# Optimization experiments

Hardware: AMD Instinct MI355X
Metric: run time of the kernel (lower is better)

## Reference

```python
import jax, jax.numpy as jnp
import numpy as np

D = 768; H = 12; T = 8; E = 4; L = 197; B = 4; BT = B * T


def _ln(x, g, b):
    m = x.mean(-1, keepdims=True)
    v = ((x - m) ** 2).mean(-1, keepdims=True)
    return (x - m) / jnp.sqrt(v + 1e-5) * g + b


def _qgelu(x):
    return x * jax.nn.sigmoid(1.702 * x)


def _mha(x, wqkv, bqkv, wo, bo):
    # x: (L, N, D), torch nn.MultiheadAttention semantics (seq-first)
    Lx, N, Dm = x.shape
    hd = Dm // H
    qkv = x @ wqkv.T + bqkv                      # (L, N, 3D)
    q, k, v = jnp.split(qkv, 3, axis=-1)
    sh = lambda t: t.reshape(Lx, N, H, hd).transpose(1, 2, 0, 3)  # (N,H,L,hd)
    q, k, v = sh(q), sh(k), sh(v)
    att = jax.nn.softmax(jnp.einsum('nhld,nhmd->nhlm', q, k) / np.sqrt(hd).astype(np.float32), -1)
    o = jnp.einsum('nhlm,nhmd->nhld', att, v).transpose(2, 0, 1, 3).reshape(Lx, N, Dm)
    return o @ wo.T + bo


def setup_inputs() -> dict:
    key = jax.random.key(0)
    ks = iter(jax.random.split(key, 40))
    s = 0.02
    p = {}
    p['x'] = jax.random.normal(next(ks), (L, BT, D), jnp.float32)
    p['msg_fc_w'] = s * jax.random.normal(next(ks), (D, D)); p['msg_fc_b'] = jnp.zeros((D,))
    p['msg_ln_g'] = jnp.ones((D,)); p['msg_ln_b'] = jnp.zeros((D,))
    p['msg_attn_wqkv'] = s * jax.random.normal(next(ks), (3 * D, D)); p['msg_attn_bqkv'] = jnp.zeros((3 * D,))
    p['msg_attn_wo'] = s * jax.random.normal(next(ks), (D, D)); p['msg_attn_bo'] = jnp.zeros((D,))
    p['attn_wqkv'] = s * jax.random.normal(next(ks), (3 * D, D)); p['attn_bqkv'] = jnp.zeros((3 * D,))
    p['attn_wo'] = s * jax.random.normal(next(ks), (D, D)); p['attn_bo'] = jnp.zeros((D,))
    p['ln1_g'] = jnp.ones((D,)); p['ln1_b'] = jnp.zeros((D,))
    p['ln2_g'] = jnp.ones((D,)); p['ln2_b'] = jnp.zeros((D,))
    p['cfc_w'] = s * jax.random.normal(next(ks), (4 * D, D)); p['cfc_b'] = jnp.zeros((4 * D,))
    p['cproj_w'] = s * jax.random.normal(next(ks), (D, 4 * D)); p['cproj_b'] = jnp.zeros((D,))
    p['eh_w'] = s * jax.random.normal(next(ks), (E, 4 * D, D)); p['eh_b'] = jnp.zeros((E, 4 * D))
    p['et_w'] = s * jax.random.normal(next(ks), (E, D, 4 * D)); p['et_b'] = jnp.zeros((E, D))
    p['r1_w'] = s * jax.random.normal(next(ks), (E + 1, D)); p['r1_b'] = jnp.zeros((E + 1,))
    p['r2_w'] = s * jax.random.normal(next(ks), (E + 1, 4 * D)); p['r2_b'] = jnp.zeros((E + 1,))
    return p


def reference(x, msg_fc_w, msg_fc_b, msg_ln_g, msg_ln_b, msg_attn_wqkv, msg_attn_bqkv,
              msg_attn_wo, msg_attn_bo, attn_wqkv, attn_bqkv, attn_wo, attn_bo,
              ln1_g, ln1_b, ln2_g, ln2_b, cfc_w, cfc_b, cproj_w, cproj_b,
              eh_w, eh_b, et_w, et_b, r1_w, r1_b, r2_w, r2_b):
    l, bt, d = x.shape
    b = bt // T
    x4 = x.reshape(l, b, T, d)
    # message token from CLS (position 0) of each frame
    msg = x4[0] @ msg_fc_w.T + msg_fc_b          # (b, T, d)
    msg = msg.transpose(1, 0, 2)                 # (T, b, d) - attend across frames
    mln = _ln(msg, msg_ln_g, msg_ln_b)
    msg = msg + _mha(mln, msg_attn_wqkv, msg_attn_bqkv, msg_attn_wo, msg_attn_bo)
    msg_r = msg.transpose(1, 0, 2)[None]         # (1, b, T, d)
    xc = jnp.concatenate([x4, msg_r], axis=0).reshape(l + 1, bt, d)
    xc = xc + _mha(_ln(xc, ln1_g, ln1_b), attn_wqkv, attn_bqkv, attn_wo, attn_bo)
    x = xc[:l]
    ln_x = _ln(x, ln2_g, ln2_b)
    # soft-MoE head: shared c_fc is expert 0, then E expert heads
    Wh = jnp.concatenate([cfc_w[None], eh_w], 0)     # (E+1, 4D, D)
    bh = jnp.concatenate([cfc_b[None], eh_b], 0)     # (E+1, 4D)
    heads = jnp.einsum('lbd,efd->lbef', ln_x, Wh) + bh  # (l, bt, E+1, 4D)
    r1 = jax.nn.softmax(ln_x @ r1_w.T + r1_b, -1)       # (l, bt, E+1)
    oh = jnp.einsum('lbe,lbef->lbf', r1, heads)
    oh = _qgelu(oh)
    # soft-MoE tail
    Wt = jnp.concatenate([cproj_w[None], et_w], 0)   # (E+1, D, 4D)
    btl = jnp.concatenate([cproj_b[None], et_b], 0)  # (E+1, D)
    tails = jnp.einsum('lbf,edf->lbed', oh, Wt) + btl  # (l, bt, E+1, D)
    r2 = jax.nn.softmax(oh @ r2_w.T + r2_b, -1)
    out = jnp.einsum('lbe,lbed->lbd', r2, tails)
    return x + out
```

## Files before the change

kernel.cpp:

```cpp
#include <hip/hip_runtime.h>
#include <hip/hip_bf16.h>

typedef __hip_bfloat16 bf16;
typedef __attribute__((ext_vector_type(8))) short short8;
typedef __attribute__((ext_vector_type(4))) float f32x4;

__device__ __forceinline__ float b2f(bf16 v){ return __bfloat162float(v); }
__device__ __forceinline__ unsigned short f2bits(float v){
  bf16 h = __float2bfloat16(v);
  return *reinterpret_cast<unsigned short*>(&h);
}

__device__ __forceinline__ void gload16(const bf16* g, bf16* l){
  __builtin_amdgcn_global_load_lds((const __attribute__((address_space(1))) void*)g,
                                   (__attribute__((address_space(3))) void*)l, 16, 0, 0);
}

__device__ __forceinline__ void ld4(const float* p, float& a,float& b,float& c,float& d){
  float4 v = *reinterpret_cast<const float4*>(p); a=v.x; b=v.y; c=v.z; d=v.w;
}
__device__ __forceinline__ float wave_sum(float v){
  #pragma unroll
  for (int off=32; off>0; off>>=1) v += __shfl_down(v, off);
  return v;
}

__global__ __launch_bounds__(256) void prep_weights(
    const float* __restrict__ s0, const float* __restrict__ s1,
    const float* __restrict__ s2, const float* __restrict__ s3,
    const float* __restrict__ s4, const float* __restrict__ s5,
    bf16* __restrict__ d0, bf16* __restrict__ d1, bf16* __restrict__ d2,
    bf16* __restrict__ d3, bf16* __restrict__ d4, bf16* __restrict__ d5){
  long i4 = (long)blockIdx.x*256 + threadIdx.x;
  const float* s; bf16* d; long base;
  if      (i4 <  442368){ s=s0; d=d0; base=0; }
  else if (i4 <  589824){ s=s1; d=d1; base=442368; }
  else if (i4 < 1179648){ s=s2; d=d2; base=589824; }
  else if (i4 < 3538944){ s=s3; d=d3; base=1179648; }
  else if (i4 < 4128768){ s=s4; d=d4; base=3538944; }
  else                  { s=s5; d=d5; base=4128768; }
  long j = (i4 - base)*4;
  float4 v = *reinterpret_cast<const float4*>(s + j);
  d[j]   = __float2bfloat16(v.x);
  d[j+1] = __float2bfloat16(v.y);
  d[j+2] = __float2bfloat16(v.z);
  d[j+3] = __float2bfloat16(v.w);
}

__global__ __launch_bounds__(256) void prep_bias(
    const float* __restrict__ cfc_b, const float* __restrict__ eh_b,
    const float* __restrict__ cproj_b, const float* __restrict__ et_b,
    float* __restrict__ bias_h, float* __restrict__ bias_t){
  int i = blockIdx.x*256 + threadIdx.x;
  if (i < 3072)       bias_h[i] = cfc_b[i];
  else if (i < 15360) bias_h[i] = eh_b[i-3072];
  else if (i < 16128) bias_t[i-15360] = cproj_b[i-15360];
  else if (i < 19200) bias_t[i-15360] = et_b[i-16128];
}

__global__ __launch_bounds__(256) void ln_rows(const float* __restrict__ in,
    const float* __restrict__ g, const float* __restrict__ b,
    float* __restrict__ out){
  int row = blockIdx.x;
  const float* x = in + (size_t)row*768;
  float* o = out + (size_t)row*768;
  float s=0.f, s2=0.f;
  for (int d=threadIdx.x; d<768; d+=256){ float v=x[d]; s+=v; s2+=v*v; }
  s = wave_sum(s); s2 = wave_sum(s2);
  __shared__ float red[8];
  __shared__ float stat[2];
  int lane = threadIdx.x & 63, wid = threadIdx.x >> 6;
  if (lane==0){ red[wid]=s; red[4+wid]=s2; }
  __syncthreads();
  if (threadIdx.x==0){
    float S=red[0]+red[1]+red[2]+red[3];
    float S2=red[4]+red[5]+red[6]+red[7];
    float m = S*(1.f/768.f);
    float var = S2*(1.f/768.f) - m*m;
    stat[0]=m; stat[1]=rsqrtf(var + 1e-5f);
  }
  __syncthreads();
  float m=stat[0], inv=stat[1];
  for (int d=threadIdx.x; d<768; d+=256)
    o[d] = (x[d]-m)*inv*g[d] + b[d];
}

__global__ __launch_bounds__(256) void ln_rows_b(const float* __restrict__ in,
    const float* __restrict__ g, const float* __restrict__ b,
    bf16* __restrict__ out){
  int row = blockIdx.x;
  const float* x = in + (size_t)row*768;
  bf16* o = out + (size_t)row*768;
  float s=0.f, s2=0.f;
  for (int d=threadIdx.x; d<768; d+=256){ float v=x[d]; s+=v; s2+=v*v; }
  s = wave_sum(s); s2 = wave_sum(s2);
  __shared__ float red[8];
  __shared__ float stat[2];
  int lane = threadIdx.x & 63, wid = threadIdx.x >> 6;
  if (lane==0){ red[wid]=s; red[4+wid]=s2; }
  __syncthreads();
  if (threadIdx.x==0){
    float S=red[0]+red[1]+red[2]+red[3];
    float S2=red[4]+red[5]+red[6]+red[7];
    float m = S*(1.f/768.f);
    float var = S2*(1.f/768.f) - m*m;
    stat[0]=m; stat[1]=rsqrtf(var + 1e-5f);
  }
  __syncthreads();
  float m=stat[0], inv=stat[1];
  for (int d=threadIdx.x; d<768; d+=256)
    o[d] = __float2bfloat16((x[d]-m)*inv*g[d] + b[d]);
}

template<int K>
__global__ __launch_bounds__(256) void router2(const bf16* __restrict__ X,
    const float* __restrict__ W, const float* __restrict__ bias,
    float* __restrict__ out, int rows){
  int row = blockIdx.x*4 + (threadIdx.x>>6);
  int lane = threadIdx.x & 63;
  if (row >= rows) return;
  const bf16* x = X + (size_t)row*K;
  constexpr int NC = K/64;
  float xa[NC];
  #pragma unroll
  for (int c=0;c<NC;++c) xa[c] = b2f(x[c*64 + lane]);
  float lg[5];
  #pragma unroll
  for (int e=0;e<5;++e){
    const float* w = W + (size_t)e*K;
    float p=0.f;
    #pragma unroll
    for (int c=0;c<NC;++c) p += xa[c]*w[c*64 + lane];
    lg[e] = wave_sum(p);
  }
  if (lane==0){
    float mx=-1e30f;
    #pragma unroll
    for (int e=0;e<5;++e){ lg[e] += bias[e]; mx = fmaxf(mx, lg[e]); }
    float s=0.f;
    #pragma unroll
    for (int e=0;e<5;++e){ lg[e]=expf(lg[e]-mx); s+=lg[e]; }
    float inv=1.f/s;
    #pragma unroll
    for (int e=0;e<5;++e) out[(size_t)row*5+e] = lg[e]*inv;
  }
}

__global__ __launch_bounds__(64) void msg_attn(const float* __restrict__ mqkv,
    float* __restrict__ mattno){
  int bh = blockIdx.x; int b = bh/12, h = bh%12;
  __shared__ float qs[8][64], ks[8][64], vs[8][64], sc[8][8];
  int lane = threadIdx.x;
  for (int i=lane; i<512; i+=64){
    int t=i>>6, d=i&63;
    size_t base = ((size_t)(b*8+t))*2304 + h*64 + d;
    qs[t][d]=mqkv[base]; ks[t][d]=mqkv[base+768]; vs[t][d]=mqkv[base+1536];
  }
  __syncthreads();
  { int t=lane>>3, m=lane&7; float a=0.f;
    #pragma unroll
    for (int d=0;d<64;++d) a += qs[t][d]*ks[m][d];
    sc[t][m] = a*0.125f; }
  __syncthreads();
  if (lane<8){
    int t=lane; float mx=-1e30f;
    #pragma unroll
    for (int m=0;m<8;++m) mx=fmaxf(mx, sc[t][m]);
    float s=0.f;
    #pragma unroll
    for (int m=0;m<8;++m){ float e=expf(sc[t][m]-mx); sc[t][m]=e; s+=e; }
    float inv=1.f/s;
    #pragma unroll
    for (int m=0;m<8;++m) sc[t][m]*=inv;
  }
  __syncthreads();
  { int t=lane>>3, d0=(lane&7)*8;
    for (int dd=0; dd<8; ++dd){
      int d=d0+dd; float a=0.f;
      #pragma unroll
      for (int m=0;m<8;++m) a += sc[t][m]*vs[m][d];
      mattno[((size_t)(b*8+t))*768 + h*64 + d] = a;
    } }
}

__global__ __launch_bounds__(256) void attn_mfma(const bf16* __restrict__ qkv,
    bf16* __restrict__ attno){
  constexpr int KP = 232;
  __shared__ __align__(16) unsigned short Ks[208*72];
  __shared__ __align__(16) unsigned short Vt[64*KP];
  __shared__ __align__(16) unsigned short Ps[4*16*KP];

  int tid = threadIdx.x;
  int bh = blockIdx.x; int bb = bh/12, h = bh%12;
  int l0 = blockIdx.y*64;
  int wv = tid>>6, ln = tid&63, quad = ln>>4, mrow = ln&15;

  for (int i=tid; i<1584; i+=256){
    int m=i>>3, dc=(i&7)<<3;
    const uint4 kv = *reinterpret_cast<const uint4*>(qkv + ((size_t)(m*32+bb))*2304 + 768 + h*64 + dc);
    *reinterpret_cast<uint4*>(Ks + m*72 + dc) = kv;
    const uint4 vv = *reinterpret_cast<const uint4*>(qkv + ((size_t)(m*32+bb))*2304 + 1536 + h*64 + dc);
    unsigned int w[4] = {vv.x, vv.y, vv.z, vv.w};
    #pragma unroll
    for (int j=0;j<4;++j){
      Vt[(dc+2*j  )*KP + m] = (unsigned short)(w[j] & 0xffff);
      Vt[(dc+2*j+1)*KP + m] = (unsigned short)(w[j] >> 16);
    }
  }
  for (int i=tid; i<10*72; i+=256) Ks[198*72 + i] = 0;
  for (int i=tid; i<64*34; i+=256){ int d=i/34, c=198+(i%34); Vt[d*KP+c] = 0; }
  { unsigned int* pz = reinterpret_cast<unsigned int*>(Ps);
    for (int i=tid; i<4*16*KP/2; i+=256) pz[i] = 0; }

  int ql = l0 + wv*16 + mrow;
  short8 aq[2] = { {0,0,0,0,0,0,0,0}, {0,0,0,0,0,0,0,0} };
  if (ql < 198){
    aq[0] = *reinterpret_cast<const short8*>(qkv + ((size_t)(ql*32+bb))*2304 + h*64 + quad*8);
    aq[1] = *reinterpret_cast<const short8*>(qkv + ((size_t)(ql*32+bb))*2304 + h*64 + 32 + quad*8);
  }
  __syncthreads();

  f32x4 sc[13];
  const f32x4 zero = {0.f,0.f,0.f,0.f};
  #pragma unroll
  for (int t=0;t<13;++t){
    const short8 bk0 = *reinterpret_cast<const short8*>(Ks + (t*16+mrow)*72 + quad*8);
    const short8 bk1 = *reinterpret_cast<const short8*>(Ks + (t*16+mrow)*72 + 32 + quad*8);
    f32x4 a = zero;
    a = __builtin_amdgcn_mfma_f32_16x16x32_bf16(aq[0], bk0, a, 0,0,0);
    a = __builtin_amdgcn_mfma_f32_16x16x32_bf16(aq[1], bk1, a, 0,0,0);
    sc[t] = a * 0.125f;
  }
  if (192 + mrow >= 198) sc[12] = (f32x4){-1e30f,-1e30f,-1e30f,-1e30f};

  float inv[4];
  #pragma unroll
  for (int r=0;r<4;++r){
    float m = -1e30f;
    #pragma unroll
    for (int t=0;t<13;++t) m = fmaxf(m, sc[t][r]);
    #pragma unroll
    for (int msk=1; msk<16; msk<<=1) m = fmaxf(m, __shfl_xor(m, msk));
    float s = 0.f;
    #pragma unroll
    for (int t=0;t<13;++t){ float e = __expf(sc[t][r]-m); sc[t][r]=e; s+=e; }
    #pragma unroll
    for (int msk=1; msk<16; msk<<=1) s += __shfl_xor(s, msk);
    inv[r] = 1.f/s;
  }

  #pragma unroll
  for (int t=0;t<13;++t)
    #pragma unroll
    for (int r=0;r<4;++r)
      Ps[(wv*16 + quad*4+r)*KP + t*16+mrow] = f2bits(sc[t][r]);
  __syncthreads();

  f32x4 o[4] = {zero,zero,zero,zero};
  #pragma unroll
  for (int kc=0;kc<7;++kc){
    const short8 ap = *reinterpret_cast<const short8*>(Ps + (wv*16+mrow)*KP + kc*32 + quad*8);
    #pragma unroll
    for (int nt=0;nt<4;++nt){
      const short8 bv = *reinterpret_cast<const short8*>(Vt + (nt*16+mrow)*KP + kc*32 + quad*8);
      o[nt] = __builtin_amdgcn_mfma_f32_16x16x32_bf16(ap, bv, o[nt], 0,0,0);
    }
  }
  #pragma unroll
  for (int r=0;r<4;++r){
    int l = l0 + wv*16 + quad*4 + r;
    if (l >= 198) continue;
    #pragma unroll
    for (int nt=0;nt<4;++nt){
      int d = nt*16 + mrow;
      attno[((size_t)(l*32+bb))*768 + h*64 + d] = __float2bfloat16(o[nt][r]*inv[r]);
    }
  }
}

__global__ __launch_bounds__(256) void gemm_nt(const float* __restrict__ A,
    const float* __restrict__ B, const float* __restrict__ bias,
    const float* res, float* C,
    int M, int N, int K){
  __shared__ __align__(16) float As[16][68];
  __shared__ __align__(16) float Bs[16][68];
  int tid=threadIdx.x, tx=tid&15, ty=tid>>4;
  int row0=blockIdx.y*64, col0=blockIdx.x*64;
  int lrow=tid>>2, lk4=(tid&3)*4;
  float acc[4][4]={};
  for (int kb=0; kb<K; kb+=16){
    int gr = row0 + lrow;
    if (gr < M){
      float a0,a1,a2,a3; ld4(A + (size_t)gr*K + kb + lk4, a0,a1,a2,a3);
      As[lk4][lrow]=a0; As[lk4+1][lrow]=a1; As[lk4+2][lrow]=a2; As[lk4+3][lrow]=a3;
    } else {
      As[lk4][lrow]=0.f; As[lk4+1][lrow]=0.f; As[lk4+2][lrow]=0.f; As[lk4+3][lrow]=0.f;
    }
    { float c0,c1,c2,c3; ld4(B + (size_t)(col0+lrow)*K + kb + lk4, c0,c1,c2,c3);
      Bs[lk4][lrow]=c0; Bs[lk4+1][lrow]=c1; Bs[lk4+2][lrow]=c2; Bs[lk4+3][lrow]=c3; }
    __syncthreads();
    #pragma unroll
    for (int kk=0;kk<16;++kk){
      float4 a4 = *reinterpret_cast<const float4*>(&As[kk][ty*4]);
      float4 b4 = *reinterpret_cast<const float4*>(&Bs[kk][tx*4]);
      float av[4]={a4.x,a4.y,a4.z,a4.w};
      float bw[4]={b4.x,b4.y,b4.z,b4.w};
      #pragma unroll
      for (int u=0;u<4;++u)
        #pragma unroll
        for (int v=0;v<4;++v) acc[u][v] += av[u]*bw[v];
    }
    __syncthreads();
  }
  #pragma unroll
  for (int u=0;u<4;++u){
    int gi = row0 + ty*4 + u;
    if (gi >= M) continue;
    #pragma unroll
    for (int v=0;v<4;++v){
      int gj = col0 + tx*4 + v;
      float r = res ? res[(size_t)gi*N+gj] : 0.f;
      float bb = bias ? bias[gj] : 0.f;
      C[(size_t)gi*N+gj] = r + acc[u][v] + bb;
    }
  }
}

template<int MODE>
__global__ __launch_bounds__(256,3) void gemm_mfma(
    const bf16* __restrict__ A, const bf16* __restrict__ B,
    const float* __restrict__ bias,
    const float* res, float* __restrict__ outf,
    bf16* __restrict__ outb, int M, int N, int K)
{
  __shared__ __align__(16) bf16 As0[4096];
  __shared__ __align__(16) bf16 As1[4096];
  __shared__ __align__(16) bf16 Bs0[4096];
  __shared__ __align__(16) bf16 Bs1[4096];

  int tid=threadIdx.x, wv=tid>>6, ln=tid&63;
  int quad=ln>>4, mrow=ln&15;
  int row0=blockIdx.y*128, col0=blockIdx.x*128;
  int wr=wv>>1, wc=wv&1;

  int c0 = wv*64 + ln;
  int r0 = c0>>2, cc=(c0&3)*8;

  int aoff[4], boff[4];
  #pragma unroll
  for (int i=0;i<4;++i){
    aoff[i] = (wr*64 + i*16 + mrow)*32 + quad*8;
    boff[i] = (wc*64 + i*16 + mrow)*32 + quad*8;
  }

  f32x4 acc[4][4];
  const f32x4 zero = {0.f,0.f,0.f,0.f};
  #pragma unroll
  for (int i=0;i<4;++i)
    #pragma unroll
    for (int j=0;j<4;++j) acc[i][j]=zero;

  const bf16* Ab = A + (size_t)(row0+r0)*K + cc;
  const bf16* Bb = B + (size_t)(col0+r0)*K + cc;
  for (int kb=0; kb<K; kb+=64){
    gload16(Ab + kb,                As0 + wv*512);
    gload16(Ab + (size_t)64*K + kb, As0 + 2048 + wv*512);
    gload16(Bb + kb,                Bs0 + wv*512);
    gload16(Bb + (size_t)64*K + kb, Bs0 + 2048 + wv*512);
    gload16(Ab + kb + 32,                As1 + wv*512);
    gload16(Ab + (size_t)64*K + kb + 32, As1 + 2048 + wv*512);
    gload16(Bb + kb + 32,                Bs1 + wv*512);
    gload16(Bb + (size_t)64*K + kb + 32, Bs1 + 2048 + wv*512);
    __syncthreads();
    short8 af[4], bfr[4];
    #pragma unroll
    for (int i=0;i<4;++i) af[i]  = *reinterpret_cast<const short8*>(As0 + aoff[i]);
    #pragma unroll
    for (int j=0;j<4;++j) bfr[j] = *reinterpret_cast<const short8*>(Bs0 + boff[j]);
    #pragma unroll
    for (int i=0;i<4;++i)
      #pragma unroll
      for (int j=0;j<4;++j)
        acc[i][j] = __builtin_amdgcn_mfma_f32_16x16x32_bf16(af[i], bfr[j], acc[i][j], 0, 0, 0);
    #pragma unroll
    for (int i=0;i<4;++i) af[i]  = *reinterpret_cast<const short8*>(As1 + aoff[i]);
    #pragma unroll
    for (int j=0;j<4;++j) bfr[j] = *reinterpret_cast<const short8*>(Bs1 + boff[j]);
    #pragma unroll
    for (int i=0;i<4;++i)
      #pragma unroll
      for (int j=0;j<4;++j)
        acc[i][j] = __builtin_amdgcn_mfma_f32_16x16x32_bf16(af[i], bfr[j], acc[i][j], 0, 0, 0);
    __syncthreads();
  }

  #pragma unroll
  for (int i=0;i<4;++i){
    #pragma unroll
    for (int r=0;r<4;++r){
      int gi = row0 + wr*64 + i*16 + quad*4 + r;
      if (gi >= M) continue;
      #pragma unroll
      for (int j=0;j<4;++j){
        int gj = col0 + wc*64 + j*16 + mrow;
        if (MODE==0) outb[(size_t)gi*N+gj] = __float2bfloat16(acc[i][j][r] + bias[gj]);
        else         outf[(size_t)gi*N+gj] = acc[i][j][r] + bias[gj] + res[(size_t)gi*N+gj];
      }
    }
  }
}

template<int MODE>
__global__ __launch_bounds__(256,2) void gemm_moe(
    const bf16* __restrict__ A, const bf16* __restrict__ B,
    const float* __restrict__ bias, const float* __restrict__ rmat,
    const float* __restrict__ res, float* __restrict__ outf,
    bf16* __restrict__ outb, int M, int N, int K)
{
  __shared__ __align__(16) bf16 As0[4096];
  __shared__ __align__(16) bf16 As1[4096];
  __shared__ __align__(16) bf16 Bs0[4096];
  __shared__ __align__(16) bf16 Bs1[4096];

  int tid=threadIdx.x, wv=tid>>6, ln=tid&63;
  int quad=ln>>4, mrow=ln&15;
  int row0=blockIdx.y*128, col0=blockIdx.x*128;
  int wr=wv>>1, wc=wv&1;

  int c0 = wv*64 + ln;
  int r0 = c0>>2, cc=(c0&3)*8;

  int aoff[4], boff[4];
  #pragma unroll
  for (int i=0;i<4;++i){
    aoff[i] = (wr*64 + i*16 + mrow)*32 + quad*8;
    boff[i] = (wc*64 + i*16 + mrow)*32 + quad*8;
  }

  const f32x4 zero = {0.f,0.f,0.f,0.f};
  f32x4 fin[4][4];
  #pragma unroll
  for (int i=0;i<4;++i)
    #pragma unroll
    for (int j=0;j<4;++j) fin[i][j]=zero;

  const bf16* Ab = A + (size_t)(row0+r0)*K + cc;

  for (int e=0; e<5; ++e){
    f32x4 acc[4][4];
    #pragma unroll
    for (int i=0;i<4;++i)
      #pragma unroll
      for (int j=0;j<4;++j) acc[i][j]=zero;

    const bf16* Bb = B + (size_t)e*N*K + (size_t)(col0+r0)*K + cc;
    for (int kb=0; kb<K; kb+=64){
      gload16(Ab + kb,                As0 + wv*512);
      gload16(Ab + (size_t)64*K + kb, As0 + 2048 + wv*512);
      gload16(Bb + kb,                Bs0 + wv*512);
      gload16(Bb + (size_t)64*K + kb, Bs0 + 2048 + wv*512);
      gload16(Ab + kb + 32,                As1 + wv*512);
      gload16(Ab + (size_t)64*K + kb + 32, As1 + 2048 + wv*512);
      gload16(Bb + kb + 32,                Bs1 + wv*512);
      gload16(Bb + (size_t)64*K + kb + 32, Bs1 + 2048 + wv*512);
      __syncthreads();
      short8 af[4], bfr[4];
      #pragma unroll
      for (int i=0;i<4;++i) af[i]  = *reinterpret_cast<const short8*>(As0 + aoff[i]);
      #pragma unroll
      for (int j=0;j<4;++j) bfr[j] = *reinterpret_cast<const short8*>(Bs0 + boff[j]);
      #pragma unroll
      for (int i=0;i<4;++i)
        #pragma unroll
        for (int j=0;j<4;++j)
          acc[i][j] = __builtin_amdgcn_mfma_f32_16x16x32_bf16(af[i], bfr[j], acc[i][j], 0, 0, 0);
      #pragma unroll
      for (int i=0;i<4;++i) af[i]  = *reinterpret_cast<const short8*>(As1 + aoff[i]);
      #pragma unroll
      for (int j=0;j<4;++j) bfr[j] = *reinterpret_cast<const short8*>(Bs1 + boff[j]);
      #pragma unroll
      for (int i=0;i<4;++i)
        #pragma unroll
        for (int j=0;j<4;++j)
          acc[i][j] = __builtin_amdgcn_mfma_f32_16x16x32_bf16(af[i], bfr[j], acc[i][j], 0, 0, 0);
      __syncthreads();
    }

    float bv[4];
    #pragma unroll
    for (int j=0;j<4;++j) bv[j] = bias[e*N + col0 + wc*64 + j*16 + mrow];
    #pragma unroll
    for (int i=0;i<4;++i){
      #pragma unroll
      for (int r=0;r<4;++r){
        int gi = row0 + wr*64 + i*16 + quad*4 + r;
        float w = (gi < M) ? rmat[(size_t)gi*5 + e] : 0.f;
        #pragma unroll
        for (int j=0;j<4;++j)
          fin[i][j][r] += w * (acc[i][j][r] + bv[j]);
      }
    }
  }

  #pragma unroll
  for (int i=0;i<4;++i){
    #pragma unroll
    for (int r=0;r<4;++r){
      int gi = row0 + wr*64 + i*16 + quad*4 + r;
      if (gi >= M) continue;
      #pragma unroll
      for (int j=0;j<4;++j){
        int gj = col0 + wc*64 + j*16 + mrow;
        float v = fin[i][j][r];
        if (MODE==0){
          float q = v / (1.f + __expf(-1.702f*v));
          outb[(size_t)gi*N+gj] = __float2bfloat16(q);
        } else {
          outf[(size_t)gi*N+gj] = v + res[(size_t)gi*N+gj];
        }
      }
    }
  }
}

extern "C" void kernel_launch(void* const* d_in, const int* in_sizes, int n_in,
                              void* d_out, int out_size, void* d_ws, size_t ws_size,
                              hipStream_t stream) {
  const float* x         = (const float*)d_in[0];
  const float* msg_fc_w  = (const float*)d_in[1];
  const float* msg_fc_b  = (const float*)d_in[2];
  const float* msg_ln_g  = (const float*)d_in[3];
  const float* msg_ln_b  = (const float*)d_in[4];
  const float* msg_wqkv  = (const float*)d_in[5];
  const float* msg_bqkv  = (const float*)d_in[6];
  const float* msg_wo    = (const float*)d_in[7];
  const float* msg_bo    = (const float*)d_in[8];
  const float* attn_wqkv = (const float*)d_in[9];
  const float* attn_bqkv = (const float*)d_in[10];
  const float* attn_wo   = (const float*)d_in[11];
  const float* attn_bo   = (const float*)d_in[12];
  const float* ln1_g     = (const float*)d_in[13];
  const float* ln1_b     = (const float*)d_in[14];
  const float* ln2_g     = (const float*)d_in[15];
  const float* ln2_b     = (const float*)d_in[16];
  const float* cfc_w     = (const float*)d_in[17];
  const float* cfc_b     = (const float*)d_in[18];
  const float* cproj_w   = (const float*)d_in[19];
  const float* cproj_b   = (const float*)d_in[20];
  const float* eh_w      = (const float*)d_in[21];
  const float* eh_b      = (const float*)d_in[22];
  const float* et_w      = (const float*)d_in[23];
  const float* et_b      = (const float*)d_in[24];
  const float* r1_w      = (const float*)d_in[25];
  const float* r1_b      = (const float*)d_in[26];
  const float* r2_w      = (const float*)d_in[27];
  const float* r2_b      = (const float*)d_in[28];
  float* out = (float*)d_out;

  float* ws     = (float*)d_ws;
  float* xc     = ws;
  float* bigA   = xc + 4866048;
  bf16*  qkv_b  = (bf16*)bigA;
  bf16*  oh_b   = (bf16*)bigA;
  float* lnbf   = bigA + 9830400;
  bf16*  lnb_b  = (bf16*)lnbf;
  float* attnof = lnbf + 2457600;
  bf16*  attno_b= (bf16*)attnof;
  float* wqf    = attnof + 2457600;
  bf16*  wq_b   = (bf16*)wqf;
  float* wof    = wqf + 884736;
  bf16*  wo_b   = (bf16*)wof;
  float* whf    = wof + 294912;
  bf16*  wh_b   = (bf16*)whf;
  float* wtf    = whf + 5898240;
  bf16*  wt_b   = (bf16*)wtf;
  float* bias_h = wtf + 5898240;
  float* bias_t = bias_h + 15360;
  float* r1b    = bias_t + 3840;
  float* r2b    = r1b + 32000;
  float* msg    = r2b + 32000;
  float* mln    = msg + 24576;
  float* mqkv   = mln + 24576;
  float* matt   = mqkv + 73728;

  prep_weights<<<dim3(6488064/256), 256, 0, stream>>>(
      attn_wqkv, attn_wo, cfc_w, eh_w, cproj_w, et_w,
      wq_b, wo_b, wh_b, wh_b + 2359296, wt_b, wt_b + 2359296);
  prep_bias<<<dim3(75), 256, 0, stream>>>(cfc_b, eh_b, cproj_b, et_b, bias_h, bias_t);

  hipMemcpyAsync(xc, x, (size_t)4841472*sizeof(float), hipMemcpyDeviceToDevice, stream);
  gemm_nt<<<dim3(12,1), 256, 0, stream>>>(x, msg_fc_w, msg_fc_b, nullptr, msg, 32, 768, 768);
  ln_rows<<<dim3(32), 256, 0, stream>>>(msg, msg_ln_g, msg_ln_b, mln);
  gemm_nt<<<dim3(36,1), 256, 0, stream>>>(mln, msg_wqkv, msg_bqkv, nullptr, mqkv, 32, 2304, 768);
  msg_attn<<<dim3(48), 64, 0, stream>>>(mqkv, matt);
  gemm_nt<<<dim3(12,1), 256, 0, stream>>>(matt, msg_wo, msg_bo, msg, xc + (size_t)6304*768, 32, 768, 768);
  ln_rows_b<<<dim3(6336), 256, 0, stream>>>(xc, ln1_g, ln1_b, lnb_b);
  gemm_mfma<0><<<dim3(18,50), 256, 0, stream>>>(lnb_b, wq_b, attn_bqkv, nullptr, nullptr, qkv_b, 6336, 2304, 768);
  attn_mfma<<<dim3(384,4), 256, 0, stream>>>(qkv_b, attno_b);
  gemm_mfma<1><<<dim3(6,50), 256, 0, stream>>>(attno_b, wo_b, attn_bo, xc, xc, nullptr, 6336, 768, 768);
  ln_rows_b<<<dim3(6304), 256, 0, stream>>>(xc, ln2_g, ln2_b, lnb_b);
  router2<768><<<dim3(1576), 256, 0, stream>>>(lnb_b, r1_w, r1_b, r1b, 6304);
  gemm_moe<0><<<dim3(24,50), 256, 0, stream>>>(lnb_b, wh_b, bias_h, r1b, nullptr, nullptr, oh_b, 6304, 3072, 768);
  router2<3072><<<dim3(1576), 256, 0, stream>>>(oh_b, r2_w, r2_b, r2b, 6304);
  gemm_moe<1><<<dim3(6,50), 256, 0, stream>>>(oh_b, wt_b, bias_t, r2b, xc, out, nullptr, 6304, 768, 3072);
}
```

Baseline: 1.085 ms.

## Shrink MoE GEMM tiles to 64x128 with XCD-aware block swizzle

Each MoE GEMM block now covers a 64x128 tile instead of 128x128. Each wave owns a 64x32 slice, which halves the accumulator registers, and launch bounds are raised to allow 3 blocks per CU. Launch is now a 1D grid whose block index is remapped so that consecutive tiles land on the same XCD, which should improve L2 reuse. The aims are more blocks for better occupancy and wave balance, especially for the tail GEMM that only had 300 blocks, at the cost of less A/B reuse per block and more global loads.

```diff
diff --git a/kernel.cpp b/kernel.cpp
--- a/kernel.cpp
+++ b/kernel.cpp
@@ -23,6 +23,12 @@
   #pragma unroll
   for (int off=32; off>0; off>>=1) v += __shfl_down(v, off);
   return v;
+}
+
+__device__ __forceinline__ int xcd_swz(int wg, int nwg){
+  int q = nwg >> 3, r = nwg & 7;
+  int x = wg & 7, i = wg >> 3;
+  return (x < r ? x*(q+1) : r*(q+1) + (x-r)*q) + i;
 }
 
 __global__ __launch_bounds__(256) void prep_weights(
@@ -411,92 +417,91 @@
 }
 
 template<int MODE>
-__global__ __launch_bounds__(256,2) void gemm_moe(
+__global__ __launch_bounds__(256,3) void gemm_moe2(
     const bf16* __restrict__ A, const bf16* __restrict__ B,
     const float* __restrict__ bias, const float* __restrict__ rmat,
     const float* __restrict__ res, float* __restrict__ outf,
     bf16* __restrict__ outb, int M, int N, int K)
 {
-  __shared__ __align__(16) bf16 As0[4096];
-  __shared__ __align__(16) bf16 As1[4096];
+  __shared__ __align__(16) bf16 As0[2048];
+  __shared__ __align__(16) bf16 As1[2048];
   __shared__ __align__(16) bf16 Bs0[4096];
   __shared__ __align__(16) bf16 Bs1[4096];
 
   int tid=threadIdx.x, wv=tid>>6, ln=tid&63;
   int quad=ln>>4, mrow=ln&15;
-  int row0=blockIdx.y*128, col0=blockIdx.x*128;
-  int wr=wv>>1, wc=wv&1;
-
-  int c0 = wv*64 + ln;
-  int r0 = c0>>2, cc=(c0&3)*8;
-
-  int aoff[4], boff[4];
-  #pragma unroll
-  for (int i=0;i<4;++i){
-    aoff[i] = (wr*64 + i*16 + mrow)*32 + quad*8;
-    boff[i] = (wc*64 + i*16 + mrow)*32 + quad*8;
-  }
+
+  int gy = (M + 63) >> 6;
+  int lin = xcd_swz(blockIdx.x, gridDim.x);
+  int bx = lin / gy, by = lin % gy;
+  int row0 = by*64, col0 = bx*128;
+
+  int r0 = tid>>2, cc=(tid&3)*8;
+
+  int aoff[4], boff[2];
+  #pragma unroll
+  for (int i=0;i<4;++i) aoff[i] = (i*16 + mrow)*32 + quad*8;
+  #pragma unroll
+  for (int j=0;j<2;++j) boff[j] = (wv*32 + j*16 + mrow)*32 + quad*8;
 
   const f32x4 zero = {0.f,0.f,0.f,0.f};
-  f32x4 fin[4][4];
+  f32x4 fin[4][2];
   #pragma unroll
   for (int i=0;i<4;++i)
     #pragma unroll
-    for (int j=0;j<4;++j) fin[i][j]=zero;
+    for (int j=0;j<2;++j) fin[i][j]=zero;
 
   const bf16* Ab = A + (size_t)(row0+r0)*K + cc;
 
   for (int e=0; e<5; ++e){
-    f32x4 acc[4][4];
+    f32x4 acc[4][2];
     #pragma unroll
     for (int i=0;i<4;++i)
       #pragma unroll
-      for (int j=0;j<4;++j) acc[i][j]=zero;
+      for (int j=0;j<2;++j) acc[i][j]=zero;
 
     const bf16* Bb = B + (size_t)e*N*K + (size_t)(col0+r0)*K + cc;
     for (int kb=0; kb<K; kb+=64){
-      gload16(Ab + kb,                As0 + wv*512);
-      gload16(Ab + (size_t)64*K + kb, As0 + 2048 + wv*512);
-      gload16(Bb + kb,                Bs0 + wv*512);
-      gload16(Bb + (size_t)64*K + kb, Bs0 + 2048 + wv*512);
+      gload16(Ab + kb,                  As0 + wv*512);
+      gload16(Bb + kb,                  Bs0 + wv*512);
+      gload16(Bb + (size_t)64*K + kb,   Bs0 + 2048 + wv*512);
       gload16(Ab + kb + 32,                As1 + wv*512);
-      gload16(Ab + (size_t)64*K + kb + 32, As1 + 2048 + wv*512);
       gload16(Bb + kb + 32,                Bs1 + wv*512);
       gload16(Bb + (size_t)64*K + kb + 32, Bs1 + 2048 + wv*512);
       __syncthreads();
-      short8 af[4], bfr[4];
+      short8 af[4], bfr[2];
       #pragma unroll
       for (int i=0;i<4;++i) af[i]  = *reinterpret_cast<const short8*>(As0 + aoff[i]);
       #pragma unroll
-      for (int j=0;j<4;++j) bfr[j] = *reinterpret_cast<const short8*>(Bs0 + boff[j]);
+      for (int j=0;j<2;++j) bfr[j] = *reinterpret_cast<const short8*>(Bs0 + boff[j]);
       #pragma unroll
       for (int i=0;i<4;++i)
         #pragma unroll
-        for (int j=0;j<4;++j)
+        for (int j=0;j<2;++j)
           acc[i][j] = __builtin_amdgcn_mfma_f32_16x16x32_bf16(af[i], bfr[j], acc[i][j], 0, 0, 0);
       #pragma unroll
       for (int i=0;i<4;++i) af[i]  = *reinterpret_cast<const short8*>(As1 + aoff[i]);
       #pragma unroll
-      for (int j=0;j<4;++j) bfr[j] = *reinterpret_cast<const short8*>(Bs1 + boff[j]);
+      for (int j=0;j<2;++j) bfr[j] = *reinterpret_cast<const short8*>(Bs1 + boff[j]);
       #pragma unroll
       for (int i=0;i<4;++i)
         #pragma unroll
-        for (int j=0;j<4;++j)
+        for (int j=0;j<2;++j)
           acc[i][j] = __builtin_amdgcn_mfma_f32_16x16x32_bf16(af[i], bfr[j], acc[i][j], 0, 0, 0);
       __syncthreads();
     }
 
-    float bv[4];
-    #pragma unroll
-    for (int j=0;j<4;++j) bv[j] = bias[e*N + col0 + wc*64 + j*16 + mrow];
+    float bv[2];
+    #pragma unroll
+    for (int j=0;j<2;++j) bv[j] = bias[e*N + col0 + wv*32 + j*16 + mrow];
     #pragma unroll
     for (int i=0;i<4;++i){
       #pragma unroll
       for (int r=0;r<4;++r){
-        int gi = row0 + wr*64 + i*16 + quad*4 + r;
+        int gi = row0 + i*16 + quad*4 + r;
         float w = (gi < M) ? rmat[(size_t)gi*5 + e] : 0.f;
         #pragma unroll
-        for (int j=0;j<4;++j)
+        for (int j=0;j<2;++j)
           fin[i][j][r] += w * (acc[i][j][r] + bv[j]);
       }
     }
@@ -506,11 +511,11 @@
   for (int i=0;i<4;++i){
     #pragma unroll
     for (int r=0;r<4;++r){
-      int gi = row0 + wr*64 + i*16 + quad*4 + r;
+      int gi = row0 + i*16 + quad*4 + r;
       if (gi >= M) continue;
       #pragma unroll
-      for (int j=0;j<4;++j){
-        int gj = col0 + wc*64 + j*16 + mrow;
+      for (int j=0;j<2;++j){
+        int gj = col0 + wv*32 + j*16 + mrow;
         float v = fin[i][j][r];
         if (MODE==0){
           float q = v / (1.f + __expf(-1.702f*v));
@@ -600,7 +605,7 @@
   gemm_mfma<1><<<dim3(6,50), 256, 0, stream>>>(attno_b, wo_b, attn_bo, xc, xc, nullptr, 6336, 768, 768);
   ln_rows_b<<<dim3(6304), 256, 0, stream>>>(xc, ln2_g, ln2_b, lnb_b);
   router2<768><<<dim3(1576), 256, 0, stream>>>(lnb_b, r1_w, r1_b, r1b, 6304);
-  gemm_moe<0><<<dim3(24,50), 256, 0, stream>>>(lnb_b, wh_b, bias_h, r1b, nullptr, nullptr, oh_b, 6304, 3072, 768);
+  gemm_moe2<0><<<dim3(24*99), 256, 0, stream>>>(lnb_b, wh_b, bias_h, r1b, nullptr, nullptr, oh_b, 6304, 3072, 768);
   router2<3072><<<dim3(1576), 256, 0, stream>>>(oh_b, r2_w, r2_b, r2b, 6304);
-  gemm_moe<1><<<dim3(6,50), 256, 0, stream>>>(oh_b, wt_b, bias_t, r2b, xc, out, nullptr, 6304, 768, 3072);
-}
+  gemm_moe2<1><<<dim3(6*99), 256, 0, stream>>>(oh_b, wt_b, bias_t, r2b, xc, out, nullptr, 6304, 768, 3072);
+}
```

Result: slower. 1.134 ms (+4.5%).

## Split-K MoE tail GEMM with atomics, double-buffer LDS, XCD-aware tile swizzle

Applied to the files above, without the earlier changes.

Rewrites the MoE GEMM as a flattened expert×K tile stream. Each workgroup can process a slice of that stream, so the tail GEMM, which has only 300 output tiles, is split three ways along K and combined with float atomicAdd. A separate init kernel writes residual plus router-weighted bias before the atomic accumulation. The kernel also double-buffers LDS with a single barrier per K step and remaps block IDs so neighbouring tiles land on the same XCD. This should raise occupancy for the under-filled tail GEMM and hide load latency, at the cost of atomic traffic, an extra kernel pass over the output, and summation order that is no longer deterministic.

```diff
diff --git a/kernel.cpp b/kernel.cpp
--- a/kernel.cpp
+++ b/kernel.cpp
@@ -23,6 +23,12 @@
   #pragma unroll
   for (int off=32; off>0; off>>=1) v += __shfl_down(v, off);
   return v;
+}
+
+__device__ __forceinline__ int xcd_swz(int wg, int nwg){
+  int q = nwg >> 3, r = nwg & 7;
+  int x = wg & 7, i = wg >> 3;
+  return (x < r ? x*(q+1) : r*(q+1) + (x-r)*q) + i;
 }
 
 __global__ __launch_bounds__(256) void prep_weights(
@@ -410,23 +416,40 @@
   }
 }
 
+__global__ __launch_bounds__(256) void tail_init(const float* __restrict__ xc,
+    const float* __restrict__ r2, const float* __restrict__ bias_t,
+    float* __restrict__ out){
+  int idx = blockIdx.x*256 + threadIdx.x;
+  if (idx >= 6304*192) return;
+  int m = idx/192, n4 = (idx%192)*4;
+  const float* rp = r2 + (size_t)m*5;
+  float4 s = *reinterpret_cast<const float4*>(xc + (size_t)m*768 + n4);
+  #pragma unroll
+  for (int e=0;e<5;++e){
+    float w = rp[e];
+    float4 b = *reinterpret_cast<const float4*>(bias_t + e*768 + n4);
+    s.x += w*b.x; s.y += w*b.y; s.z += w*b.z; s.w += w*b.w;
+  }
+  *reinterpret_cast<float4*>(out + (size_t)m*768 + n4) = s;
+}
+
 template<int MODE>
-__global__ __launch_bounds__(256,2) void gemm_moe(
+__global__ __launch_bounds__(256,2) void gemm_moe4(
     const bf16* __restrict__ A, const bf16* __restrict__ B,
-    const float* __restrict__ bias, const float* __restrict__ rmat,
-    const float* __restrict__ res, float* __restrict__ outf,
-    bf16* __restrict__ outb, int M, int N, int K)
+    const float* __restrict__ biasH, const float* __restrict__ rmat,
+    float* __restrict__ outf, bf16* __restrict__ outb,
+    int M, int N, int K0, int totTiles, int TZ)
 {
-  __shared__ __align__(16) bf16 As0[4096];
-  __shared__ __align__(16) bf16 As1[4096];
-  __shared__ __align__(16) bf16 Bs0[4096];
-  __shared__ __align__(16) bf16 Bs1[4096];
+  __shared__ __align__(16) bf16 As[2][2][4096];
+  __shared__ __align__(16) bf16 Bs[2][2][4096];
 
   int tid=threadIdx.x, wv=tid>>6, ln=tid&63;
   int quad=ln>>4, mrow=ln&15;
-  int row0=blockIdx.y*128, col0=blockIdx.x*128;
+  int gy = (M + 127) >> 7;
+  int lin = xcd_swz(blockIdx.x, gridDim.x);
+  int bx = lin / gy, by = lin % gy;
+  int row0 = by*128, col0 = bx*128;
   int wr=wv>>1, wc=wv&1;
-
   int c0 = wv*64 + ln;
   int r0 = c0>>2, cc=(c0&3)*8;
 
@@ -438,69 +461,83 @@
   }
 
   const f32x4 zero = {0.f,0.f,0.f,0.f};
-  f32x4 fin[4][4];
+  f32x4 acc[4][4], fin[4][4];
   #pragma unroll
   for (int i=0;i<4;++i)
     #pragma unroll
-    for (int j=0;j<4;++j) fin[i][j]=zero;
-
-  const bf16* Ab = A + (size_t)(row0+r0)*K + cc;
-
-  for (int e=0; e<5; ++e){
-    f32x4 acc[4][4];
+    for (int j=0;j<4;++j){ acc[i][j]=zero; fin[i][j]=zero; }
+
+  int t0 = blockIdx.y * TZ;
+  int nt = totTiles - t0; if (nt > TZ) nt = TZ;
+  int tpe = K0 >> 6;
+  int es = t0 / tpe, ks = (t0 - es*tpe) << 6;
+  int ec = es,       kc = ks;
+
+  const bf16* Abase = A + (size_t)(row0+r0)*K0 + cc;
+
+#define MOE_STAGE(buf) { \
+    const bf16* Ap = Abase + ks; \
+    const bf16* Bp = B + ((size_t)es*N + col0 + r0)*K0 + ks + cc; \
+    gload16(Ap,                   &As[buf][0][wv*512]); \
+    gload16(Ap + (size_t)64*K0,   &As[buf][0][2048 + wv*512]); \
+    gload16(Ap + 32,              &As[buf][1][wv*512]); \
+    gload16(Ap + (size_t)64*K0+32,&As[buf][1][2048 + wv*512]); \
+    gload16(Bp,                   &Bs[buf][0][wv*512]); \
+    gload16(Bp + (size_t)64*K0,   &Bs[buf][0][2048 + wv*512]); \
+    gload16(Bp + 32,              &Bs[buf][1][wv*512]); \
+    gload16(Bp + (size_t)64*K0+32,&Bs[buf][1][2048 + wv*512]); \
+    ks += 64; if (ks == K0){ ks = 0; ++es; } }
+
+  MOE_STAGE(0);
+  __syncthreads();
+
+  int cur = 0;
+  for (int t=0; t<nt; ++t){
+    if (t+1 < nt){ MOE_STAGE(cur^1); }
+    short8 af[4], bfr[4];
+    #pragma unroll
+    for (int i=0;i<4;++i) af[i]  = *reinterpret_cast<const short8*>(&As[cur][0][aoff[i]]);
+    #pragma unroll
+    for (int j=0;j<4;++j) bfr[j] = *reinterpret_cast<const short8*>(&Bs[cur][0][boff[j]]);
     #pragma unroll
     for (int i=0;i<4;++i)
       #pragma unroll
-      for (int j=0;j<4;++j) acc[i][j]=zero;
-
-    const bf16* Bb = B + (size_t)e*N*K + (size_t)(col0+r0)*K + cc;
-    for (int kb=0; kb<K; kb+=64){
-      gload16(Ab + kb,                As0 + wv*512);
-      gload16(Ab + (size_t)64*K + kb, As0 + 2048 + wv*512);
-      gload16(Bb + kb,                Bs0 + wv*512);
-      gload16(Bb + (size_t)64*K + kb, Bs0 + 2048 + wv*512);
-      gload16(Ab + kb + 32,                As1 + wv*512);
-      gload16(Ab + (size_t)64*K + kb + 32, As1 + 2048 + wv*512);
-      gload16(Bb + kb + 32,                Bs1 + wv*512);
-      gload16(Bb + (size_t)64*K + kb + 32, Bs1 + 2048 + wv*512);
-      __syncthreads();
-      short8 af[4], bfr[4];
-      #pragma unroll
-      for (int i=0;i<4;++i) af[i]  = *reinterpret_cast<const short8*>(As0 + aoff[i]);
-      #pragma unroll
-      for (int j=0;j<4;++j) bfr[j] = *reinterpret_cast<const short8*>(Bs0 + boff[j]);
+      for (int j=0;j<4;++j)
+        acc[i][j] = __builtin_amdgcn_mfma_f32_16x16x32_bf16(af[i], bfr[j], acc[i][j], 0, 0, 0);
+    #pragma unroll
+    for (int i=0;i<4;++i) af[i]  = *reinterpret_cast<const short8*>(&As[cur][1][aoff[i]]);
+    #pragma unroll
+    for (int j=0;j<4;++j) bfr[j] = *reinterpret_cast<const short8*>(&Bs[cur][1][boff[j]]);
+    #pragma unroll
+    for (int i=0;i<4;++i)
+      #pragma unroll
+      for (int j=0;j<4;++j)
+        acc[i][j] = __builtin_amdgcn_mfma_f32_16x16x32_bf16(af[i], bfr[j], acc[i][j], 0, 0, 0);
+
+    kc += 64;
+    if (kc == K0 || t == nt-1){
+      #pragma unroll
+      for (int i=0;i<4;++i){
+        #pragma unroll
+        for (int r=0;r<4;++r){
+          int gi = row0 + wr*64 + i*16 + quad*4 + r;
+          if (gi < M){
+            float w = rmat[(size_t)gi*5 + ec];
+            #pragma unroll
+            for (int j=0;j<4;++j) fin[i][j][r] += w*acc[i][j][r];
+          }
+        }
+      }
       #pragma unroll
       for (int i=0;i<4;++i)
         #pragma unroll
-        for (int j=0;j<4;++j)
-          acc[i][j] = __builtin_amdgcn_mfma_f32_16x16x32_bf16(af[i], bfr[j], acc[i][j], 0, 0, 0);
-      #pragma unroll
-      for (int i=0;i<4;++i) af[i]  = *reinterpret_cast<const short8*>(As1 + aoff[i]);
-      #pragma unroll
-      for (int j=0;j<4;++j) bfr[j] = *reinterpret_cast<const short8*>(Bs1 + boff[j]);
-      #pragma unroll
-      for (int i=0;i<4;++i)
-        #pragma unroll
-        for (int j=0;j<4;++j)
-          acc[i][j] = __builtin_amdgcn_mfma_f32_16x16x32_bf16(af[i], bfr[j], acc[i][j], 0, 0, 0);
-      __syncthreads();
-    }
-
-    float bv[4];
-    #pragma unroll
-    for (int j=0;j<4;++j) bv[j] = bias[e*N + col0 + wc*64 + j*16 + mrow];
-    #pragma unroll
-    for (int i=0;i<4;++i){
-      #pragma unroll
-      for (int r=0;r<4;++r){
-        int gi = row0 + wr*64 + i*16 + quad*4 + r;
-        float w = (gi < M) ? rmat[(size_t)gi*5 + e] : 0.f;
-        #pragma unroll
-        for (int j=0;j<4;++j)
-          fin[i][j][r] += w * (acc[i][j][r] + bv[j]);
-      }
-    }
-  }
+        for (int j=0;j<4;++j) acc[i][j]=zero;
+      kc = 0; ++ec;
+    }
+    __syncthreads();
+    cur ^= 1;
+  }
+#undef MOE_STAGE
 
   #pragma unroll
   for (int i=0;i<4;++i){
@@ -508,15 +545,18 @@
     for (int r=0;r<4;++r){
       int gi = row0 + wr*64 + i*16 + quad*4 + r;
       if (gi >= M) continue;
+      const float* rp = rmat + (size_t)gi*5;
       #pragma unroll
       for (int j=0;j<4;++j){
         int gj = col0 + wc*64 + j*16 + mrow;
         float v = fin[i][j][r];
         if (MODE==0){
+          #pragma unroll
+          for (int e=0;e<5;++e) v += rp[e]*biasH[(size_t)e*N + gj];
           float q = v / (1.f + __expf(-1.702f*v));
           outb[(size_t)gi*N+gj] = __float2bfloat16(q);
         } else {
-          outf[(size_t)gi*N+gj] = v + res[(size_t)gi*N+gj];
+          atomicAdd(&outf[(size_t)gi*N+gj], v);
         }
       }
     }
@@ -600,7 +640,8 @@
   gemm_mfma<1><<<dim3(6,50), 256, 0, stream>>>(attno_b, wo_b, attn_bo, xc, xc, nullptr, 6336, 768, 768);
   ln_rows_b<<<dim3(6304), 256, 0, stream>>>(xc, ln2_g, ln2_b, lnb_b);
   router2<768><<<dim3(1576), 256, 0, stream>>>(lnb_b, r1_w, r1_b, r1b, 6304);
-  gemm_moe<0><<<dim3(24,50), 256, 0, stream>>>(lnb_b, wh_b, bias_h, r1b, nullptr, nullptr, oh_b, 6304, 3072, 768);
+  gemm_moe4<0><<<dim3(24*50, 1), 256, 0, stream>>>(lnb_b, wh_b, bias_h, r1b, nullptr, oh_b, 6304, 3072, 768, 60, 60);
   router2<3072><<<dim3(1576), 256, 0, stream>>>(oh_b, r2_w, r2_b, r2b, 6304);
-  gemm_moe<1><<<dim3(6,50), 256, 0, stream>>>(oh_b, wt_b, bias_t, r2b, xc, out, nullptr, 6304, 768, 3072);
-}
+  tail_init<<<dim3((6304*192+255)/256), 256, 0, stream>>>(xc, r2b, bias_t, out);
+  gemm_moe4<1><<<dim3(6*50, 3), 256, 0, stream>>>(oh_b, wt_b, nullptr, r2b, out, nullptr, 6304, 768, 3072, 240, 80);
+}
```

After: 997.8 us. 8.0% less time.
